# Optimization experiments

Measured on AMD Instinct MI355X. Metric: run time of the kernel, lower is better.

## Reference

```python
import jax, jax.numpy as jnp
import numpy as np

B = 256      # batch
D_IN = 784   # input_dims
WIDTH = 256  # block width
DEPTH = 10   # number of fc_relu blocks
NCLS = 10    # num_classes


def setup_inputs() -> dict:
    key = jax.random.key(0)
    ks = jax.random.split(key, 7)
    s1 = 1.0 / np.sqrt(D_IN)
    s2 = 1.0 / np.sqrt(WIDTH)
    x = jax.random.normal(ks[0], (B, D_IN), jnp.float32)
    W1 = jax.random.uniform(ks[1], (WIDTH, D_IN), jnp.float32, -s1, s1)
    b1 = jax.random.uniform(ks[2], (WIDTH,), jnp.float32, -s1, s1)
    Wb = jax.random.uniform(ks[3], (DEPTH, WIDTH, WIDTH), jnp.float32, -s2, s2)
    bb = jax.random.uniform(ks[4], (DEPTH, WIDTH), jnp.float32, -s2, s2)
    Wl = jax.random.uniform(ks[5], (NCLS, WIDTH), jnp.float32, -s2, s2)
    bl = jax.random.uniform(ks[6], (NCLS,), jnp.float32, -s2, s2)
    return dict(x=x, W1=W1, b1=b1, Wb=Wb, bb=bb, Wl=Wl, bl=bl)


def reference(x, W1, b1, Wb, bb, Wl, bl):
    # first_fc + relu
    y = jax.nn.relu(x @ W1.T + b1)                      # [B, WIDTH]
    eye = jnp.eye(WIDTH, dtype=y.dtype)

    def step(y, wb):
        W, b = wb                                       # [WIDTH, WIDTH], [WIDTH]
        # fc_relu.dev(x, skip=True): per-sample Jacobian W @ diag(relu'(x)) + I
        # (W @ diag(d) scales columns of W by d) -- vectorized replacement for
        # the original nested Python-loop diag build.
        mask = (y >= 0).astype(y.dtype)                 # [B, WIDTH]
        J = W[None, :, :] * mask[:, None, :] + eye      # [B, WIDTH, WIDTH]
        sigma = jnp.linalg.svd(J, compute_uv=False)     # [B, WIDTH], descending
        # residual relu block: relu(fc(x)) + x
        y = jax.nn.relu(y @ W.T + b) + y
        return y, sigma

    y, sigmas = jax.lax.scan(step, y, (Wb, bb))         # sigmas: [DEPTH, B, WIDTH]
    # feat_tag='ldi': all_sigma = mean over blocks of sigma_mean
    all_sigma = jnp.mean(sigmas, axis=0)                # [B, WIDTH]
    out = y @ Wl.T + bl                                 # last_fc, [B, NCLS]
    return out, all_sigma
```

## Files before the change

### kernel.cpp

```cpp
#include <hip/hip_runtime.h>
#include <hip/hip_bf16.h>

#define NW 256
#define NDEPTH 10
#define NS 25
#define PAD 12
#define PIV_EPS 1e-6f

__global__ __launch_bounds__(256) void forward_kernel(
    const float* __restrict__ x, const float* __restrict__ W1, const float* __restrict__ b1,
    const float* __restrict__ Wb, const float* __restrict__ bb,
    const float* __restrict__ Wl, const float* __restrict__ bl,
    float* __restrict__ out) {
  const int b = blockIdx.x;
  const int o = threadIdx.x;
  __shared__ __align__(16) float xs[784];
  __shared__ __align__(16) float ybuf[2][NW];

  for (int k = o; k < 784; k += 256) xs[k] = x[(size_t)b * 784 + k];
  __syncthreads();

  {
    const float* w1r = W1 + (size_t)o * 784;
    float s = b1[o];
    for (int k = 0; k < 784; k += 4) {
      float4 w = *(const float4*)(w1r + k);
      float4 xv = *(const float4*)(&xs[k]);
      s += w.x * xv.x + w.y * xv.y + w.z * xv.z + w.w * xv.w;
    }
    ybuf[0][o] = fmaxf(s, 0.f);
  }
  __syncthreads();

  int cur = 0;
  for (int d = 0; d < NDEPTH; ++d) {
    const float* wr = Wb + (size_t)d * NW * NW + (size_t)o * NW;
    const float* yc = ybuf[cur];
    float acc = bb[d * NW + o];
#pragma unroll 8
    for (int k = 0; k < NW; k += 4) {
      float4 w = *(const float4*)(wr + k);
      float4 yv = *(const float4*)(&yc[k]);
      acc += w.x * yv.x + w.y * yv.y + w.z * yv.z + w.w * yv.w;
    }
    float ynew = fmaxf(acc, 0.f) + yc[o];
    ybuf[cur ^ 1][o] = ynew;
    __syncthreads();
    cur ^= 1;
  }

  if (o < 10) {
    const float* wr = Wl + o * NW;
    const float* yc = ybuf[cur];
    float acc = bl[o];
    for (int k = 0; k < NW; k += 4) {
      float4 w = *(const float4*)(wr + k);
      float4 yv = *(const float4*)(&yc[k]);
      acc += w.x * yv.x + w.y * yv.y + w.z * yv.z + w.w * yv.w;
    }
    out[b * 10 + o] = acc;
  }
}

__global__ void bmat_kernel(const float* __restrict__ Wb, float* __restrict__ Ball,
                            unsigned int* __restrict__ rsmax) {
  const int blk = blockIdx.x;
  const int k   = blk >> 5;
  const int r0  = (blk & 31) << 3;
  const int c   = threadIdx.x;
  const float* W = Wb + (size_t)k * NW * NW;
  float acc[8] = {0.f,0.f,0.f,0.f,0.f,0.f,0.f,0.f};
  for (int j = 0; j < NW; ++j) {
    const float wc = W[j * NW + c];
#pragma unroll
    for (int rr = 0; rr < 8; ++rr) acc[rr] += wc * W[j * NW + r0 + rr];
  }
  float a[8];
#pragma unroll
  for (int rr = 0; rr < 8; ++rr) {
    const int r = r0 + rr;
    const float s = acc[rr] + W[c * NW + r] + W[r * NW + c] + ((r == c) ? 1.f : 0.f);
    Ball[(size_t)k * NW * NW + r * NW + c] = s;
    a[rr] = fabsf(s);
  }
  __shared__ float wsum[4][8];
#pragma unroll
  for (int off = 32; off; off >>= 1) {
#pragma unroll
    for (int rr = 0; rr < 8; ++rr) a[rr] += __shfl_down(a[rr], off);
  }
  if ((c & 63) == 0) {
#pragma unroll
    for (int rr = 0; rr < 8; ++rr) wsum[c >> 6][rr] = a[rr];
  }
  __syncthreads();
  if (c == 0) {
    float mx = 0.f;
#pragma unroll
    for (int rr = 0; rr < 8; ++rr) {
      const float s = wsum[0][rr] + wsum[1][rr] + wsum[2][rr] + wsum[3][rr];
      mx = fmaxf(mx, s);
    }
    atomicMax(&rsmax[k], __float_as_uint(mx));
  }
}

__global__ __launch_bounds__(1024, 4) void ldl_kernel(const float* __restrict__ Ball,
                                                      const unsigned int* __restrict__ rsmax,
                                                      int* __restrict__ counts) {
  const int s   = blockIdx.x;
  const int mat = blockIdx.y;
  const int t = threadIdx.x;
  const int l = t & 63;
  const int w = t >> 6;
  const int rg = l & 31;
  const int ch = 2 * w + (l >> 5);
  const int r0 = rg << 3;

  __shared__ __align__(16) float vrow[2][2][32 * PAD];

  const float h = sqrtf(__uint_as_float(rsmax[mat])) * (1.f / NS);
  const float sg = (s + 1) * h;
  const float mu = sg * sg;

  float Bf[64];
  {
    const float* src = Ball + (size_t)mat * NW * NW + (size_t)r0 * NW + (ch << 3);
#pragma unroll
    for (int i = 0; i < 8; ++i) {
      const float4 a = *(const float4*)(src + i * NW);
      const float4 b = *(const float4*)(src + i * NW + 4);
      Bf[i*8+0] = a.x; Bf[i*8+1] = a.y; Bf[i*8+2] = a.z; Bf[i*8+3] = a.w;
      Bf[i*8+4] = b.x; Bf[i*8+5] = b.y; Bf[i*8+6] = b.z; Bf[i*8+7] = b.w;
    }
  }
  if (rg == ch) {
#pragma unroll
    for (int i = 0; i < 8; ++i) Bf[i*8+i] -= mu;
  }

  if (rg == 0) {
    float* vd0 = &vrow[0][0][ch * PAD];
    float* vd1 = &vrow[0][1][ch * PAD];
    *(float4*)&vd0[0] = make_float4(Bf[0],  Bf[1],  Bf[2],  Bf[3]);
    *(float4*)&vd0[4] = make_float4(Bf[4],  Bf[5],  Bf[6],  Bf[7]);
    *(float4*)&vd1[0] = make_float4(Bf[8],  Bf[9],  Bf[10], Bf[11]);
    *(float4*)&vd1[4] = make_float4(Bf[12], Bf[13], Bf[14], Bf[15]);
  }
  __syncthreads();

  int cnt = 0;
  for (int m = 0; m < NW / 2; ++m) {
    const int k = 2 * m;
    const int par = m & 1;
    const float* v0 = vrow[par][0];
    const float* v1 = vrow[par][1];

    const int kpos = (k >> 3) * PAD + (k & 7);
    const float2 p01 = *(const float2*)&v0[kpos];
    const float d0  = p01.x;
    const float u01 = p01.y;
    const float e1  = v1[kpos + 1];
    const float d0g = (fabsf(d0) < PIV_EPS) ? copysignf(PIV_EPS, d0) : d0;
    const float i0  = __builtin_amdgcn_rcpf(d0g);
    const float l10 = u01 * i0;
    const float d1  = e1 - l10 * u01;
    const float d1g = (fabsf(d1) < PIV_EPS) ? copysignf(PIV_EPS, d1) : d1;
    const float i1  = __builtin_amdgcn_rcpf(d1g);
    cnt += (d0 < 0.f) ? 1 : 0;
    cnt += (d1 < 0.f) ? 1 : 0;

    if (16 * w + 15 > k) {
      const float4 ra0 = *(const float4*)&v0[rg * PAD + 0];
      const float4 ra1 = *(const float4*)&v0[rg * PAD + 4];
      const float4 rb0 = *(const float4*)&v1[rg * PAD + 0];
      const float4 rb1 = *(const float4*)&v1[rg * PAD + 4];
      const float4 ca0 = *(const float4*)&v0[ch * PAD + 0];
      const float4 ca1 = *(const float4*)&v0[ch * PAD + 4];
      const float4 cb0 = *(const float4*)&v1[ch * PAD + 0];
      const float4 cb1 = *(const float4*)&v1[ch * PAD + 4];
      const float rv0[8] = {ra0.x, ra0.y, ra0.z, ra0.w, ra1.x, ra1.y, ra1.z, ra1.w};
      const float rv1[8] = {rb0.x, rb0.y, rb0.z, rb0.w, rb1.x, rb1.y, rb1.z, rb1.w};
      const float cv0[8] = {ca0.x, ca0.y, ca0.z, ca0.w, ca1.x, ca1.y, ca1.z, ca1.w};
      const float cv1[8] = {cb0.x, cb0.y, cb0.z, cb0.w, cb1.x, cb1.y, cb1.z, cb1.w};

      float g0[8], f1[8];
#pragma unroll
      for (int i = 0; i < 8; ++i) {
        const int r = r0 + i;
        const float f0 = (r > k)     ? -rv0[i] * i0 : 0.f;
        const float v1p = rv1[i] - l10 * rv0[i];
        f1[i] = (r > k + 1) ? -v1p * i1 : 0.f;
        g0[i] = f0 - l10 * f1[i];
      }
#pragma unroll
      for (int i = 0; i < 8; ++i) {
#pragma unroll
        for (int j = 0; j < 8; ++j) {
          Bf[i*8+j] = fmaf(g0[i], cv0[j], fmaf(f1[i], cv1[j], Bf[i*8+j]));
        }
      }
      const int nr = k + 2;
      if (nr < NW && rg == (nr >> 3)) {
        float* vd0 = &vrow[par ^ 1][0][ch * PAD];
        float* vd1 = &vrow[par ^ 1][1][ch * PAD];
        switch (nr & 7) {
          case 0:
            *(float4*)&vd0[0] = make_float4(Bf[0],  Bf[1],  Bf[2],  Bf[3]);
            *(float4*)&vd0[4] = make_float4(Bf[4],  Bf[5],  Bf[6],  Bf[7]);
            *(float4*)&vd1[0] = make_float4(Bf[8],  Bf[9],  Bf[10], Bf[11]);
            *(float4*)&vd1[4] = make_float4(Bf[12], Bf[13], Bf[14], Bf[15]);
            break;
          case 2:
            *(float4*)&vd0[0] = make_float4(Bf[16], Bf[17], Bf[18], Bf[19]);
            *(float4*)&vd0[4] = make_float4(Bf[20], Bf[21], Bf[22], Bf[23]);
            *(float4*)&vd1[0] = make_float4(Bf[24], Bf[25], Bf[26], Bf[27]);
            *(float4*)&vd1[4] = make_float4(Bf[28], Bf[29], Bf[30], Bf[31]);
            break;
          case 4:
            *(float4*)&vd0[0] = make_float4(Bf[32], Bf[33], Bf[34], Bf[35]);
            *(float4*)&vd0[4] = make_float4(Bf[36], Bf[37], Bf[38], Bf[39]);
            *(float4*)&vd1[0] = make_float4(Bf[40], Bf[41], Bf[42], Bf[43]);
            *(float4*)&vd1[4] = make_float4(Bf[44], Bf[45], Bf[46], Bf[47]);
            break;
          default:
            *(float4*)&vd0[0] = make_float4(Bf[48], Bf[49], Bf[50], Bf[51]);
            *(float4*)&vd0[4] = make_float4(Bf[52], Bf[53], Bf[54], Bf[55]);
            *(float4*)&vd1[0] = make_float4(Bf[56], Bf[57], Bf[58], Bf[59]);
            *(float4*)&vd1[4] = make_float4(Bf[60], Bf[61], Bf[62], Bf[63]);
            break;
        }
      }
    }
    __syncthreads();
  }

  if (t == 0) counts[mat * NS + s] = cnt;
}

__global__ void gather_kernel(const int* __restrict__ counts,
                              const unsigned int* __restrict__ rsmax,
                              float* __restrict__ sigw) {
  const int mat = blockIdx.x;
  const int j = threadIdx.x;
  __shared__ int cs[NS];
  if (j < NS) cs[j] = counts[mat * NS + j];
  __syncthreads();
  const float h = sqrtf(__uint_as_float(rsmax[mat])) * (1.f / NS);
  int cmax = 0;
  int sstar = NS - 1;
  bool found = false;
  for (int s = 0; s < NS; ++s) {
    cmax = max(cmax, cs[s]);
    if (!found && cmax > j) { sstar = s; found = true; }
  }
  sigw[mat * NW + (255 - j)] = (sstar + 0.5f) * h;
}

__global__ void sig_avg_kernel(const float* __restrict__ sig, float* __restrict__ out_all) {
  const int b = blockIdx.x;
  const int j = threadIdx.x;
  float s = 0.f;
#pragma unroll
  for (int k = 0; k < NDEPTH; ++k) s += sig[k * NW + j];
  out_all[b * NW + j] = s * 0.1f;
}

extern "C" void kernel_launch(void* const* d_in, const int* in_sizes, int n_in,
                              void* d_out, int out_size, void* d_ws, size_t ws_size,
                              hipStream_t stream) {
  const float* x  = (const float*)d_in[0];
  const float* W1 = (const float*)d_in[1];
  const float* b1 = (const float*)d_in[2];
  const float* Wb = (const float*)d_in[3];
  const float* bb = (const float*)d_in[4];
  const float* Wl = (const float*)d_in[5];
  const float* bl = (const float*)d_in[6];
  float* out = (float*)d_out;

  float* ws = (float*)d_ws;
  float* Ball   = ws;
  float* sigw   = ws + 655360;
  unsigned int* rsmaxW = (unsigned int*)(ws + 657920);
  int*   counts = (int*)(ws + 657936);

  hipMemsetAsync(rsmaxW, 0, NDEPTH * sizeof(unsigned int), stream);
  bmat_kernel<<<dim3(NDEPTH * 32), dim3(256), 0, stream>>>(Wb, Ball, rsmaxW);
  forward_kernel<<<dim3(256), dim3(256), 0, stream>>>(x, W1, b1, Wb, bb, Wl, bl, out);
  ldl_kernel<<<dim3(NS, NDEPTH), dim3(1024), 0, stream>>>(Ball, rsmaxW, counts);
  gather_kernel<<<dim3(NDEPTH), dim3(256), 0, stream>>>(counts, rsmaxW, sigw);
  sig_avg_kernel<<<dim3(256), dim3(256), 0, stream>>>(sigw, out + 2560);
}
```

Measured before the change: 286.2 us.

## Block LDL elimination by 4 pivots, fuse bmat with forward, fuse gather kernels

The LDL inertia-count kernel now eliminates four pivots per step instead of two, using a small 4x4 block factorisation. That halves the number of barrier-separated iterations and gives larger FMA bursts per shared-memory load. The B-matrix build and the forward MLP are merged into one launch with split block roles, and the gather and sigma-averaging kernels are combined into one, dropping launches and a workspace round trip. The forward dot products also use multiple accumulators for ILP. The cost is more register pressure in the LDL kernel and some redundant per-block recomputation in the fused gather.

```diff
diff --git a/kernel.cpp b/kernel.cpp
--- a/kernel.cpp
+++ b/kernel.cpp
@@ -7,101 +7,117 @@
 #define PAD 12
 #define PIV_EPS 1e-6f
 
-__global__ __launch_bounds__(256) void forward_kernel(
+__global__ __launch_bounds__(256) void bmat_fwd_kernel(
+    const float* __restrict__ Wb, float* __restrict__ Ball, unsigned int* __restrict__ rsmax,
     const float* __restrict__ x, const float* __restrict__ W1, const float* __restrict__ b1,
-    const float* __restrict__ Wb, const float* __restrict__ bb,
-    const float* __restrict__ Wl, const float* __restrict__ bl,
+    const float* __restrict__ bb, const float* __restrict__ Wl, const float* __restrict__ bl,
     float* __restrict__ out) {
-  const int b = blockIdx.x;
-  const int o = threadIdx.x;
   __shared__ __align__(16) float xs[784];
   __shared__ __align__(16) float ybuf[2][NW];
-
-  for (int k = o; k < 784; k += 256) xs[k] = x[(size_t)b * 784 + k];
-  __syncthreads();
-
-  {
-    const float* w1r = W1 + (size_t)o * 784;
-    float s = b1[o];
-    for (int k = 0; k < 784; k += 4) {
-      float4 w = *(const float4*)(w1r + k);
-      float4 xv = *(const float4*)(&xs[k]);
-      s += w.x * xv.x + w.y * xv.y + w.z * xv.z + w.w * xv.w;
-    }
-    ybuf[0][o] = fmaxf(s, 0.f);
-  }
-  __syncthreads();
-
-  int cur = 0;
-  for (int d = 0; d < NDEPTH; ++d) {
-    const float* wr = Wb + (size_t)d * NW * NW + (size_t)o * NW;
-    const float* yc = ybuf[cur];
-    float acc = bb[d * NW + o];
-#pragma unroll 8
-    for (int k = 0; k < NW; k += 4) {
-      float4 w = *(const float4*)(wr + k);
-      float4 yv = *(const float4*)(&yc[k]);
-      acc += w.x * yv.x + w.y * yv.y + w.z * yv.z + w.w * yv.w;
-    }
-    float ynew = fmaxf(acc, 0.f) + yc[o];
-    ybuf[cur ^ 1][o] = ynew;
+  __shared__ float wsum[4][8];
+
+  if (blockIdx.x < NDEPTH * 32) {
+    const int blk = blockIdx.x;
+    const int k   = blk >> 5;
+    const int r0  = (blk & 31) << 3;
+    const int c   = threadIdx.x;
+    const float* W = Wb + (size_t)k * NW * NW;
+    float acc[8] = {0.f,0.f,0.f,0.f,0.f,0.f,0.f,0.f};
+    for (int j = 0; j < NW; ++j) {
+      const float wc = W[j * NW + c];
+#pragma unroll
+      for (int rr = 0; rr < 8; ++rr) acc[rr] += wc * W[j * NW + r0 + rr];
+    }
+    float a[8];
+#pragma unroll
+    for (int rr = 0; rr < 8; ++rr) {
+      const int r = r0 + rr;
+      const float s = acc[rr] + W[c * NW + r] + W[r * NW + c] + ((r == c) ? 1.f : 0.f);
+      Ball[(size_t)k * NW * NW + r * NW + c] = s;
+      a[rr] = fabsf(s);
+    }
+#pragma unroll
+    for (int off = 32; off; off >>= 1) {
+#pragma unroll
+      for (int rr = 0; rr < 8; ++rr) a[rr] += __shfl_down(a[rr], off);
+    }
+    if ((c & 63) == 0) {
+#pragma unroll
+      for (int rr = 0; rr < 8; ++rr) wsum[c >> 6][rr] = a[rr];
+    }
     __syncthreads();
-    cur ^= 1;
-  }
-
-  if (o < 10) {
-    const float* wr = Wl + o * NW;
-    const float* yc = ybuf[cur];
-    float acc = bl[o];
-    for (int k = 0; k < NW; k += 4) {
-      float4 w = *(const float4*)(wr + k);
-      float4 yv = *(const float4*)(&yc[k]);
-      acc += w.x * yv.x + w.y * yv.y + w.z * yv.z + w.w * yv.w;
-    }
-    out[b * 10 + o] = acc;
-  }
-}
-
-__global__ void bmat_kernel(const float* __restrict__ Wb, float* __restrict__ Ball,
-                            unsigned int* __restrict__ rsmax) {
-  const int blk = blockIdx.x;
-  const int k   = blk >> 5;
-  const int r0  = (blk & 31) << 3;
-  const int c   = threadIdx.x;
-  const float* W = Wb + (size_t)k * NW * NW;
-  float acc[8] = {0.f,0.f,0.f,0.f,0.f,0.f,0.f,0.f};
-  for (int j = 0; j < NW; ++j) {
-    const float wc = W[j * NW + c];
-#pragma unroll
-    for (int rr = 0; rr < 8; ++rr) acc[rr] += wc * W[j * NW + r0 + rr];
-  }
-  float a[8];
-#pragma unroll
-  for (int rr = 0; rr < 8; ++rr) {
-    const int r = r0 + rr;
-    const float s = acc[rr] + W[c * NW + r] + W[r * NW + c] + ((r == c) ? 1.f : 0.f);
-    Ball[(size_t)k * NW * NW + r * NW + c] = s;
-    a[rr] = fabsf(s);
-  }
-  __shared__ float wsum[4][8];
-#pragma unroll
-  for (int off = 32; off; off >>= 1) {
-#pragma unroll
-    for (int rr = 0; rr < 8; ++rr) a[rr] += __shfl_down(a[rr], off);
-  }
-  if ((c & 63) == 0) {
-#pragma unroll
-    for (int rr = 0; rr < 8; ++rr) wsum[c >> 6][rr] = a[rr];
-  }
-  __syncthreads();
-  if (c == 0) {
-    float mx = 0.f;
-#pragma unroll
-    for (int rr = 0; rr < 8; ++rr) {
-      const float s = wsum[0][rr] + wsum[1][rr] + wsum[2][rr] + wsum[3][rr];
-      mx = fmaxf(mx, s);
-    }
-    atomicMax(&rsmax[k], __float_as_uint(mx));
+    if (c == 0) {
+      float mx = 0.f;
+#pragma unroll
+      for (int rr = 0; rr < 8; ++rr)
+        mx = fmaxf(mx, wsum[0][rr] + wsum[1][rr] + wsum[2][rr] + wsum[3][rr]);
+      atomicMax(&rsmax[k], __float_as_uint(mx));
+    }
+  } else {
+    const int b = blockIdx.x - NDEPTH * 32;
+    const int o = threadIdx.x;
+    for (int k = o; k < 784; k += 256) xs[k] = x[(size_t)b * 784 + k];
+    __syncthreads();
+    {
+      const float* w1r = W1 + (size_t)o * 784;
+      float a0 = 0.f, a1 = 0.f, a2 = 0.f, a3 = 0.f;
+      for (int k = 0; k < 784; k += 16) {
+        const float4 w0 = *(const float4*)(w1r + k);
+        const float4 x0 = *(const float4*)(&xs[k]);
+        const float4 w1v = *(const float4*)(w1r + k + 4);
+        const float4 x1 = *(const float4*)(&xs[k + 4]);
+        const float4 w2 = *(const float4*)(w1r + k + 8);
+        const float4 x2 = *(const float4*)(&xs[k + 8]);
+        const float4 w3 = *(const float4*)(w1r + k + 12);
+        const float4 x3 = *(const float4*)(&xs[k + 12]);
+        a0 += w0.x*x0.x + w0.y*x0.y + w0.z*x0.z + w0.w*x0.w;
+        a1 += w1v.x*x1.x + w1v.y*x1.y + w1v.z*x1.z + w1v.w*x1.w;
+        a2 += w2.x*x2.x + w2.y*x2.y + w2.z*x2.z + w2.w*x2.w;
+        a3 += w3.x*x3.x + w3.y*x3.y + w3.z*x3.z + w3.w*x3.w;
+      }
+      ybuf[0][o] = fmaxf(b1[o] + ((a0 + a1) + (a2 + a3)), 0.f);
+    }
+    __syncthreads();
+    int cur = 0;
+    for (int d = 0; d < NDEPTH; ++d) {
+      const float* wr = Wb + (size_t)d * NW * NW + (size_t)o * NW;
+      const float* yc = ybuf[cur];
+      float a0 = 0.f, a1 = 0.f, a2 = 0.f, a3 = 0.f;
+#pragma unroll 4
+      for (int k = 0; k < NW; k += 16) {
+        const float4 w0 = *(const float4*)(wr + k);
+        const float4 y0 = *(const float4*)(&yc[k]);
+        const float4 w1v = *(const float4*)(wr + k + 4);
+        const float4 y1 = *(const float4*)(&yc[k + 4]);
+        const float4 w2 = *(const float4*)(wr + k + 8);
+        const float4 y2 = *(const float4*)(&yc[k + 8]);
+        const float4 w3 = *(const float4*)(wr + k + 12);
+        const float4 y3 = *(const float4*)(&yc[k + 12]);
+        a0 += w0.x*y0.x + w0.y*y0.y + w0.z*y0.z + w0.w*y0.w;
+        a1 += w1v.x*y1.x + w1v.y*y1.y + w1v.z*y1.z + w1v.w*y1.w;
+        a2 += w2.x*y2.x + w2.y*y2.y + w2.z*y2.z + w2.w*y2.w;
+        a3 += w3.x*y3.x + w3.y*y3.y + w3.z*y3.z + w3.w*y3.w;
+      }
+      const float acc = bb[d * NW + o] + ((a0 + a1) + (a2 + a3));
+      const float ynew = fmaxf(acc, 0.f) + yc[o];
+      ybuf[cur ^ 1][o] = ynew;
+      __syncthreads();
+      cur ^= 1;
+    }
+    if (o < 10) {
+      const float* wr = Wl + o * NW;
+      const float* yc = ybuf[cur];
+      float a0 = 0.f, a1 = 0.f;
+      for (int k = 0; k < NW; k += 8) {
+        const float4 w0 = *(const float4*)(wr + k);
+        const float4 y0 = *(const float4*)(&yc[k]);
+        const float4 w1v = *(const float4*)(wr + k + 4);
+        const float4 y1 = *(const float4*)(&yc[k + 4]);
+        a0 += w0.x*y0.x + w0.y*y0.y + w0.z*y0.z + w0.w*y0.w;
+        a1 += w1v.x*y1.x + w1v.y*y1.y + w1v.z*y1.z + w1v.w*y1.w;
+      }
+      out[b * 10 + o] = bl[o] + a0 + a1;
+    }
   }
 }
 
@@ -117,7 +133,7 @@
   const int ch = 2 * w + (l >> 5);
   const int r0 = rg << 3;
 
-  __shared__ __align__(16) float vrow[2][2][32 * PAD];
+  __shared__ __align__(16) float vrow[2][4][32 * PAD];
 
   const float h = sqrtf(__uint_as_float(rsmax[mat])) * (1.f / NS);
   const float sg = (s + 1) * h;
@@ -140,95 +156,117 @@
   }
 
   if (rg == 0) {
-    float* vd0 = &vrow[0][0][ch * PAD];
-    float* vd1 = &vrow[0][1][ch * PAD];
-    *(float4*)&vd0[0] = make_float4(Bf[0],  Bf[1],  Bf[2],  Bf[3]);
-    *(float4*)&vd0[4] = make_float4(Bf[4],  Bf[5],  Bf[6],  Bf[7]);
-    *(float4*)&vd1[0] = make_float4(Bf[8],  Bf[9],  Bf[10], Bf[11]);
-    *(float4*)&vd1[4] = make_float4(Bf[12], Bf[13], Bf[14], Bf[15]);
+#pragma unroll
+    for (int m4 = 0; m4 < 4; ++m4) {
+      float* vd = &vrow[0][m4][ch * PAD];
+      *(float4*)&vd[0] = make_float4(Bf[m4*8+0], Bf[m4*8+1], Bf[m4*8+2], Bf[m4*8+3]);
+      *(float4*)&vd[4] = make_float4(Bf[m4*8+4], Bf[m4*8+5], Bf[m4*8+6], Bf[m4*8+7]);
+    }
   }
   __syncthreads();
 
   int cnt = 0;
-  for (int m = 0; m < NW / 2; ++m) {
-    const int k = 2 * m;
+  for (int m = 0; m < NW / 4; ++m) {
+    const int k = 4 * m;
     const int par = m & 1;
     const float* v0 = vrow[par][0];
     const float* v1 = vrow[par][1];
+    const float* v2 = vrow[par][2];
+    const float* v3 = vrow[par][3];
 
     const int kpos = (k >> 3) * PAD + (k & 7);
-    const float2 p01 = *(const float2*)&v0[kpos];
-    const float d0  = p01.x;
-    const float u01 = p01.y;
-    const float e1  = v1[kpos + 1];
+    const float4 p0 = *(const float4*)&v0[kpos];
+    const float4 p1 = *(const float4*)&v1[kpos];
+    const float4 p2 = *(const float4*)&v2[kpos];
+    const float4 p3 = *(const float4*)&v3[kpos];
+    const float d0 = p0.x, u01 = p0.y, u02 = p0.z, u03 = p0.w;
     const float d0g = (fabsf(d0) < PIV_EPS) ? copysignf(PIV_EPS, d0) : d0;
-    const float i0  = __builtin_amdgcn_rcpf(d0g);
-    const float l10 = u01 * i0;
-    const float d1  = e1 - l10 * u01;
-    const float d1g = (fabsf(d1) < PIV_EPS) ? copysignf(PIV_EPS, d1) : d1;
-    const float i1  = __builtin_amdgcn_rcpf(d1g);
-    cnt += (d0 < 0.f) ? 1 : 0;
-    cnt += (d1 < 0.f) ? 1 : 0;
+    const float i0 = __builtin_amdgcn_rcpf(d0g);
+    const float l10 = u01 * i0, l20 = u02 * i0, l30 = u03 * i0;
+    const float e11 = p1.y - l10 * u01;
+    const float e12 = p1.z - l10 * u02;
+    const float e13 = p1.w - l10 * u03;
+    const float d1g = (fabsf(e11) < PIV_EPS) ? copysignf(PIV_EPS, e11) : e11;
+    const float i1 = __builtin_amdgcn_rcpf(d1g);
+    const float l21 = e12 * i1, l31 = e13 * i1;
+    const float e22 = p2.z - l20 * u02 - l21 * e12;
+    const float e23 = p2.w - l20 * u03 - l21 * e13;
+    const float e33a = p3.w - l30 * u03 - l31 * e13;
+    const float d2g = (fabsf(e22) < PIV_EPS) ? copysignf(PIV_EPS, e22) : e22;
+    const float i2 = __builtin_amdgcn_rcpf(d2g);
+    const float l32 = e23 * i2;
+    const float e33 = e33a - l32 * e23;
+    const float d3g = (fabsf(e33) < PIV_EPS) ? copysignf(PIV_EPS, e33) : e33;
+    const float i3 = __builtin_amdgcn_rcpf(d3g);
+    cnt += (d0 < 0.f) + (e11 < 0.f) + (e22 < 0.f) + (e33 < 0.f);
 
     if (16 * w + 15 > k) {
-      const float4 ra0 = *(const float4*)&v0[rg * PAD + 0];
-      const float4 ra1 = *(const float4*)&v0[rg * PAD + 4];
-      const float4 rb0 = *(const float4*)&v1[rg * PAD + 0];
-      const float4 rb1 = *(const float4*)&v1[rg * PAD + 4];
-      const float4 ca0 = *(const float4*)&v0[ch * PAD + 0];
-      const float4 ca1 = *(const float4*)&v0[ch * PAD + 4];
-      const float4 cb0 = *(const float4*)&v1[ch * PAD + 0];
-      const float4 cb1 = *(const float4*)&v1[ch * PAD + 4];
-      const float rv0[8] = {ra0.x, ra0.y, ra0.z, ra0.w, ra1.x, ra1.y, ra1.z, ra1.w};
-      const float rv1[8] = {rb0.x, rb0.y, rb0.z, rb0.w, rb1.x, rb1.y, rb1.z, rb1.w};
-      const float cv0[8] = {ca0.x, ca0.y, ca0.z, ca0.w, ca1.x, ca1.y, ca1.z, ca1.w};
-      const float cv1[8] = {cb0.x, cb0.y, cb0.z, cb0.w, cb1.x, cb1.y, cb1.z, cb1.w};
-
-      float g0[8], f1[8];
-#pragma unroll
-      for (int i = 0; i < 8; ++i) {
-        const int r = r0 + i;
-        const float f0 = (r > k)     ? -rv0[i] * i0 : 0.f;
-        const float v1p = rv1[i] - l10 * rv0[i];
-        f1[i] = (r > k + 1) ? -v1p * i1 : 0.f;
-        g0[i] = f0 - l10 * f1[i];
-      }
-#pragma unroll
-      for (int i = 0; i < 8; ++i) {
-#pragma unroll
-        for (int j = 0; j < 8; ++j) {
-          Bf[i*8+j] = fmaf(g0[i], cv0[j], fmaf(f1[i], cv1[j], Bf[i*8+j]));
+#pragma unroll
+      for (int ih = 0; ih < 2; ++ih) {
+        const float4 r0v = *(const float4*)&v0[rg * PAD + 4 * ih];
+        const float4 r1v = *(const float4*)&v1[rg * PAD + 4 * ih];
+        const float4 r2v = *(const float4*)&v2[rg * PAD + 4 * ih];
+        const float4 r3v = *(const float4*)&v3[rg * PAD + 4 * ih];
+        float g0[4], g1[4], g2[4], g3[4];
+#pragma unroll
+        for (int i = 0; i < 4; ++i) {
+          const int r = r0 + 4 * ih + i;
+          const float rv0 = (i == 0) ? r0v.x : (i == 1) ? r0v.y : (i == 2) ? r0v.z : r0v.w;
+          const float rv1 = (i == 0) ? r1v.x : (i == 1) ? r1v.y : (i == 2) ? r1v.z : r1v.w;
+          const float rv2 = (i == 0) ? r2v.x : (i == 1) ? r2v.y : (i == 2) ? r2v.z : r2v.w;
+          const float rv3 = (i == 0) ? r3v.x : (i == 1) ? r3v.y : (i == 2) ? r3v.z : r3v.w;
+          const float f0 = (r > k)     ? rv0 * i0 : 0.f;
+          const float a1 = rv1 - f0 * u01;
+          const float f1 = (r > k + 1) ? a1 * i1 : 0.f;
+          const float a2 = rv2 - f0 * u02 - f1 * e12;
+          const float f2 = (r > k + 2) ? a2 * i2 : 0.f;
+          const float a3 = rv3 - f0 * u03 - f1 * e13 - f2 * e23;
+          const float f3 = (r > k + 3) ? a3 * i3 : 0.f;
+          const float q3 = f3;
+          const float q2 = f2 - l32 * q3;
+          const float q1 = f1 - l21 * q2 - l31 * q3;
+          const float q0 = f0 - l10 * q1 - l20 * q2 - l30 * q3;
+          g0[i] = -q0; g1[i] = -q1; g2[i] = -q2; g3[i] = -q3;
         }
-      }
-      const int nr = k + 2;
+#pragma unroll
+        for (int jh = 0; jh < 2; ++jh) {
+          const float4 c0v = *(const float4*)&v0[ch * PAD + 4 * jh];
+          const float4 c1v = *(const float4*)&v1[ch * PAD + 4 * jh];
+          const float4 c2v = *(const float4*)&v2[ch * PAD + 4 * jh];
+          const float4 c3v = *(const float4*)&v3[ch * PAD + 4 * jh];
+#pragma unroll
+          for (int i = 0; i < 4; ++i) {
+            const int base = (4 * ih + i) * 8 + 4 * jh;
+            float b0 = Bf[base + 0], b1_ = Bf[base + 1], b2 = Bf[base + 2], b3 = Bf[base + 3];
+            b0 = fmaf(g0[i], c0v.x, b0); b1_ = fmaf(g0[i], c0v.y, b1_);
+            b2 = fmaf(g0[i], c0v.z, b2); b3 = fmaf(g0[i], c0v.w, b3);
+            b0 = fmaf(g1[i], c1v.x, b0); b1_ = fmaf(g1[i], c1v.y, b1_);
+            b2 = fmaf(g1[i], c1v.z, b2); b3 = fmaf(g1[i], c1v.w, b3);
+            b0 = fmaf(g2[i], c2v.x, b0); b1_ = fmaf(g2[i], c2v.y, b1_);
+            b2 = fmaf(g2[i], c2v.z, b2); b3 = fmaf(g2[i], c2v.w, b3);
+            b0 = fmaf(g3[i], c3v.x, b0); b1_ = fmaf(g3[i], c3v.y, b1_);
+            b2 = fmaf(g3[i], c3v.z, b2); b3 = fmaf(g3[i], c3v.w, b3);
+            Bf[base + 0] = b0; Bf[base + 1] = b1_; Bf[base + 2] = b2; Bf[base + 3] = b3;
+          }
+        }
+      }
+      const int nr = k + 4;
       if (nr < NW && rg == (nr >> 3)) {
-        float* vd0 = &vrow[par ^ 1][0][ch * PAD];
-        float* vd1 = &vrow[par ^ 1][1][ch * PAD];
-        switch (nr & 7) {
-          case 0:
-            *(float4*)&vd0[0] = make_float4(Bf[0],  Bf[1],  Bf[2],  Bf[3]);
-            *(float4*)&vd0[4] = make_float4(Bf[4],  Bf[5],  Bf[6],  Bf[7]);
-            *(float4*)&vd1[0] = make_float4(Bf[8],  Bf[9],  Bf[10], Bf[11]);
-            *(float4*)&vd1[4] = make_float4(Bf[12], Bf[13], Bf[14], Bf[15]);
-            break;
-          case 2:
-            *(float4*)&vd0[0] = make_float4(Bf[16], Bf[17], Bf[18], Bf[19]);
-            *(float4*)&vd0[4] = make_float4(Bf[20], Bf[21], Bf[22], Bf[23]);
-            *(float4*)&vd1[0] = make_float4(Bf[24], Bf[25], Bf[26], Bf[27]);
-            *(float4*)&vd1[4] = make_float4(Bf[28], Bf[29], Bf[30], Bf[31]);
-            break;
-          case 4:
-            *(float4*)&vd0[0] = make_float4(Bf[32], Bf[33], Bf[34], Bf[35]);
-            *(float4*)&vd0[4] = make_float4(Bf[36], Bf[37], Bf[38], Bf[39]);
-            *(float4*)&vd1[0] = make_float4(Bf[40], Bf[41], Bf[42], Bf[43]);
-            *(float4*)&vd1[4] = make_float4(Bf[44], Bf[45], Bf[46], Bf[47]);
-            break;
-          default:
-            *(float4*)&vd0[0] = make_float4(Bf[48], Bf[49], Bf[50], Bf[51]);
-            *(float4*)&vd0[4] = make_float4(Bf[52], Bf[53], Bf[54], Bf[55]);
-            *(float4*)&vd1[0] = make_float4(Bf[56], Bf[57], Bf[58], Bf[59]);
-            *(float4*)&vd1[4] = make_float4(Bf[60], Bf[61], Bf[62], Bf[63]);
-            break;
+        if ((nr & 7) == 0) {
+#pragma unroll
+          for (int m4 = 0; m4 < 4; ++m4) {
+            float* vd = &vrow[par ^ 1][m4][ch * PAD];
+            *(float4*)&vd[0] = make_float4(Bf[m4*8+0], Bf[m4*8+1], Bf[m4*8+2], Bf[m4*8+3]);
+            *(float4*)&vd[4] = make_float4(Bf[m4*8+4], Bf[m4*8+5], Bf[m4*8+6], Bf[m4*8+7]);
+          }
+        } else {
+#pragma unroll
+          for (int m4 = 0; m4 < 4; ++m4) {
+            float* vd = &vrow[par ^ 1][m4][ch * PAD];
+            const int ro = (m4 + 4) * 8;
+            *(float4*)&vd[0] = make_float4(Bf[ro+0], Bf[ro+1], Bf[ro+2], Bf[ro+3]);
+            *(float4*)&vd[4] = make_float4(Bf[ro+4], Bf[ro+5], Bf[ro+6], Bf[ro+7]);
+          }
         }
       }
     }
@@ -238,32 +276,25 @@
   if (t == 0) counts[mat * NS + s] = cnt;
 }
 
-__global__ void gather_kernel(const int* __restrict__ counts,
-                              const unsigned int* __restrict__ rsmax,
-                              float* __restrict__ sigw) {
-  const int mat = blockIdx.x;
-  const int j = threadIdx.x;
-  __shared__ int cs[NS];
-  if (j < NS) cs[j] = counts[mat * NS + j];
-  __syncthreads();
-  const float h = sqrtf(__uint_as_float(rsmax[mat])) * (1.f / NS);
-  int cmax = 0;
-  int sstar = NS - 1;
-  bool found = false;
-  for (int s = 0; s < NS; ++s) {
-    cmax = max(cmax, cs[s]);
-    if (!found && cmax > j) { sstar = s; found = true; }
-  }
-  sigw[mat * NW + (255 - j)] = (sstar + 0.5f) * h;
-}
-
-__global__ void sig_avg_kernel(const float* __restrict__ sig, float* __restrict__ out_all) {
+__global__ void gather_out_kernel(const int* __restrict__ counts,
+                                  const unsigned int* __restrict__ rsmax,
+                                  float* __restrict__ out_all) {
   const int b = blockIdx.x;
   const int j = threadIdx.x;
-  float s = 0.f;
-#pragma unroll
-  for (int k = 0; k < NDEPTH; ++k) s += sig[k * NW + j];
-  out_all[b * NW + j] = s * 0.1f;
+  float acc = 0.f;
+#pragma unroll
+  for (int mat = 0; mat < NDEPTH; ++mat) {
+    const float h = sqrtf(__uint_as_float(rsmax[mat])) * (1.f / NS);
+    int cmax = 0;
+    int sstar = NS - 1;
+    bool found = false;
+    for (int s = 0; s < NS; ++s) {
+      cmax = max(cmax, counts[mat * NS + s]);
+      if (!found && cmax > (255 - j)) { sstar = s; found = true; }
+    }
+    acc += (sstar + 0.5f) * h;
+  }
+  out_all[b * NW + j] = acc * 0.1f;
 }
 
 extern "C" void kernel_launch(void* const* d_in, const int* in_sizes, int n_in,
@@ -280,14 +311,12 @@
 
   float* ws = (float*)d_ws;
   float* Ball   = ws;
-  float* sigw   = ws + 655360;
-  unsigned int* rsmaxW = (unsigned int*)(ws + 657920);
-  int*   counts = (int*)(ws + 657936);
+  unsigned int* rsmaxW = (unsigned int*)(ws + 655360);
+  int*   counts = (int*)(ws + 655376);
 
   hipMemsetAsync(rsmaxW, 0, NDEPTH * sizeof(unsigned int), stream);
-  bmat_kernel<<<dim3(NDEPTH * 32), dim3(256), 0, stream>>>(Wb, Ball, rsmaxW);
-  forward_kernel<<<dim3(256), dim3(256), 0, stream>>>(x, W1, b1, Wb, bb, Wl, bl, out);
+  bmat_fwd_kernel<<<dim3(NDEPTH * 32 + 256), dim3(256), 0, stream>>>(
+      Wb, Ball, rsmaxW, x, W1, b1, bb, Wl, bl, out);
   ldl_kernel<<<dim3(NS, NDEPTH), dim3(1024), 0, stream>>>(Ball, rsmaxW, counts);
-  gather_kernel<<<dim3(NDEPTH), dim3(256), 0, stream>>>(counts, rsmaxW, sigw);
-  sig_avg_kernel<<<dim3(256), dim3(256), 0, stream>>>(sigw, out + 2560);
+  gather_out_kernel<<<dim3(256), dim3(256), 0, stream>>>(counts, rsmaxW, out + 2560);
 }
```

After: 623.6 us. 118% more time.
